# Performance work log

Hardware: AMD Instinct MI355X
Metric: run time of the kernel (lower is better)

The kernel has to match this reference:

```python
import jax, jax.numpy as jnp
import numpy as np

NUM_HEADS = 16
DIM_MODEL = 1024
DIM_K = DIM_MODEL // NUM_HEADS  # 64


def setup_inputs() -> dict:
    key = jax.random.key(0)
    ks = jax.random.split(key, 8)
    B, S, D = 2, 2048, DIM_MODEL
    scale = 1.0 / np.sqrt(D)
    return {
        "X_q": jax.random.normal(ks[0], (B, S, D), dtype=jnp.float32),
        "X_k": jax.random.normal(ks[1], (B, S, D), dtype=jnp.float32),
        "X_v": jax.random.normal(ks[2], (B, S, D), dtype=jnp.float32),
        # weights stored as [in, out] (apply as x @ W)
        "W_query": jax.random.normal(ks[3], (D, D), dtype=jnp.float32) * scale,
        "W_key": jax.random.normal(ks[4], (D, D), dtype=jnp.float32) * scale,
        "W_value": jax.random.normal(ks[5], (D, D), dtype=jnp.float32) * scale,
        "W_hidden": jax.random.normal(ks[6], (D, D), dtype=jnp.float32) * scale,
        "b_hidden": jnp.zeros((D,), dtype=jnp.float32),
    }


def _split_heads(x, B, S):
    # [B, S, D] -> [B, H, S, dk]
    return x.reshape(B, S, NUM_HEADS, DIM_K).transpose(0, 2, 1, 3)


def reference(X_q, X_k, X_v, W_query, W_key, W_value, W_hidden, b_hidden):
    B, S, D = X_q.shape
    Q = _split_heads(X_q @ W_query, B, S)
    K = _split_heads(X_k @ W_key, B, X_k.shape[1])
    V = _split_heads(X_v @ W_value, B, X_v.shape[1])
    Q = Q / np.sqrt(DIM_K).astype(np.float32)
    scores = jnp.einsum("bhqd,bhkd->bhqk", Q, K)
    A = jax.nn.sigmoid(scores)  # sigmoid attention, not softmax
    H = jnp.einsum("bhqk,bhkd->bhqd", A, V)
    # group heads: [B, H, S, dk] -> [B, S, D]
    H_cat = H.transpose(0, 2, 1, 3).reshape(B, S, D)
    H_out = H_cat @ W_hidden + b_hidden
    return (H_out, A)
```

## Files before the change

### kernel.cpp

```cpp
#include <hip/hip_runtime.h>
#include <hip/hip_bf16.h>
#include <cstddef>

typedef __bf16 bf16x8 __attribute__((ext_vector_type(8)));
typedef __bf16 bf16x4 __attribute__((ext_vector_type(4)));
typedef float f32x4 __attribute__((ext_vector_type(4)));

#define MFMA16(a, b, c) __builtin_amdgcn_mfma_f32_16x16x32_bf16((a), (b), (c), 0, 0, 0)

__global__ __launch_bounds__(256) void cvt3(const float* __restrict__ a,
                                            const float* __restrict__ b,
                                            const float* __restrict__ c,
                                            __bf16* __restrict__ oa,
                                            __bf16* __restrict__ ob,
                                            __bf16* __restrict__ oc) {
  const float* src = blockIdx.y == 0 ? a : (blockIdx.y == 1 ? b : c);
  __bf16* dst = blockIdx.y == 0 ? oa : (blockIdx.y == 1 ? ob : oc);
  const size_t i = ((size_t)blockIdx.x * 256 + threadIdx.x) * 4;
  float4 v = *(const float4*)(src + i);
  bf16x4 o = {(__bf16)v.x, (__bf16)v.y, (__bf16)v.z, (__bf16)v.w};
  *(bf16x4*)(dst + i) = o;
}

__global__ __launch_bounds__(256) void twt(const float* __restrict__ w0, const float* __restrict__ w1,
                                           const float* __restrict__ w2, const float* __restrict__ w3,
                                           __bf16* __restrict__ o0, __bf16* __restrict__ o1,
                                           __bf16* __restrict__ o2, __bf16* __restrict__ o3) {
  const float* W;
  __bf16* O;
  switch (blockIdx.z) {
    case 0: W = w0; O = o0; break;
    case 1: W = w1; O = o1; break;
    case 2: W = w2; O = o2; break;
    default: W = w3; O = o3; break;
  }
  __shared__ float t[32][33];
  const int tx = threadIdx.x & 31, ty = threadIdx.x >> 5;
  const int bx = blockIdx.x * 32, by = blockIdx.y * 32;
#pragma unroll
  for (int i = 0; i < 4; ++i)
    t[ty + 8 * i][tx] = W[(size_t)(by + ty + 8 * i) * 1024 + bx + tx];
  __syncthreads();
#pragma unroll
  for (int i = 0; i < 4; ++i)
    O[(size_t)(bx + ty + 8 * i) * 1024 + by + tx] = (__bf16)t[tx][ty + 8 * i];
}

template <bool OUT_BF16>
__global__ __launch_bounds__(256) void gemm_bt(const __bf16* __restrict__ A,
                                               const __bf16* __restrict__ B,
                                               void* __restrict__ Cout,
                                               const float* __restrict__ bias,
                                               float scale) {
  constexpr int K = 1024, N = 1024;
  const int tid = threadIdx.x, wave = tid >> 6, lane = tid & 63;
  const int qd = lane >> 4, ln = lane & 15;
  const int m0 = blockIdx.y * 128, n0 = blockIdx.x * 128;
  const int wr = wave >> 1, wc = wave & 1;

  __shared__ __align__(16) __bf16 sA[128][40];
  __shared__ __align__(16) __bf16 sB[128][40];

  f32x4 acc[4][4] = {};

  const int srow = tid >> 2, sch = (tid & 3) * 8;

  for (int k0 = 0; k0 < K; k0 += 32) {
    __syncthreads();
    *(bf16x8*)&sA[srow][sch]      = *(const bf16x8*)(A + (size_t)(m0 + srow) * K + k0 + sch);
    *(bf16x8*)&sA[srow + 64][sch] = *(const bf16x8*)(A + (size_t)(m0 + srow + 64) * K + k0 + sch);
    *(bf16x8*)&sB[srow][sch]      = *(const bf16x8*)(B + (size_t)(n0 + srow) * K + k0 + sch);
    *(bf16x8*)&sB[srow + 64][sch] = *(const bf16x8*)(B + (size_t)(n0 + srow + 64) * K + k0 + sch);
    __syncthreads();

    bf16x8 af[4], bfv[4];
#pragma unroll
    for (int i = 0; i < 4; ++i) af[i] = *(const bf16x8*)&sA[wr * 64 + i * 16 + ln][qd * 8];
#pragma unroll
    for (int j = 0; j < 4; ++j) bfv[j] = *(const bf16x8*)&sB[wc * 64 + j * 16 + ln][qd * 8];
#pragma unroll
    for (int i = 0; i < 4; ++i)
#pragma unroll
      for (int j = 0; j < 4; ++j) acc[i][j] = MFMA16(af[i], bfv[j], acc[i][j]);
  }

#pragma unroll
  for (int i = 0; i < 4; ++i)
#pragma unroll
    for (int j = 0; j < 4; ++j)
#pragma unroll
      for (int r = 0; r < 4; ++r) {
        const int row = m0 + wr * 64 + i * 16 + qd * 4 + r;
        const int col = n0 + wc * 64 + j * 16 + ln;
        float v = acc[i][j][r] * scale;
        if (bias) v += bias[col];
        if (OUT_BF16)
          ((__bf16*)Cout)[(size_t)row * N + col] = (__bf16)v;
        else
          ((float*)Cout)[(size_t)row * N + col] = v;
      }
}

__global__ __launch_bounds__(256) void attn(const __bf16* __restrict__ Q,
                                            const __bf16* __restrict__ Kb,
                                            const __bf16* __restrict__ Vb,
                                            float* __restrict__ Aout,
                                            __bf16* __restrict__ Hc) {
  const int qt = blockIdx.x, h = blockIdx.y, b = blockIdx.z;
  const int tid = threadIdx.x, wave = tid >> 6, lane = tid & 63;
  const int qd = lane >> 4, ln = lane & 15;
  const int q0 = qt * 64;
  const int wr = wave >> 1, wc = wave & 1;

  __shared__ __align__(16) __bf16 sVt[64][132];
  __shared__ __align__(16) __bf16 sKA[128 * 72];

  const __bf16* Qg = Q + (size_t)(b * 2048 + q0) * 1024 + h * 64;
  bf16x8 qf[2][2];
#pragma unroll
  for (int i = 0; i < 2; ++i)
#pragma unroll
    for (int s = 0; s < 2; ++s)
      qf[i][s] = *(const bf16x8*)(Qg + (size_t)(wr * 32 + i * 16 + ln) * 1024 + s * 32 + qd * 8);

  f32x4 hacc[4] = {};
  float* Ag = Aout + ((size_t)((b * 16 + h) * 2048 + q0)) * 2048;

  for (int kt = 0; kt < 16; ++kt) {
    const int k0 = kt * 128;
    __syncthreads();

    const __bf16* Kg = Kb + (size_t)(b * 2048 + k0) * 1024 + h * 64;
    const __bf16* Vg = Vb + (size_t)(b * 2048 + k0) * 1024 + h * 64;
#pragma unroll
    for (int p = 0; p < 4; ++p) {
      const int idx = p * 256 + tid, row = idx >> 3, ch = (idx & 7) * 8;
      *(bf16x8*)&sKA[row * 72 + ch] = *(const bf16x8*)(Kg + (size_t)row * 1024 + ch);
      bf16x8 v = *(const bf16x8*)(Vg + (size_t)row * 1024 + ch);
#pragma unroll
      for (int e = 0; e < 8; ++e) sVt[ch + e][row] = v[e];
    }
    __syncthreads();

    f32x4 sacc[2][4] = {};
#pragma unroll
    for (int ks = 0; ks < 64; ks += 32) {
      bf16x8 bfv[4];
#pragma unroll
      for (int j = 0; j < 4; ++j)
        bfv[j] = *(const bf16x8*)&sKA[(wc * 64 + j * 16 + ln) * 72 + ks + qd * 8];
#pragma unroll
      for (int i = 0; i < 2; ++i)
#pragma unroll
        for (int j = 0; j < 4; ++j) sacc[i][j] = MFMA16(qf[i][ks / 32], bfv[j], sacc[i][j]);
    }
    __syncthreads();

#pragma unroll
    for (int i = 0; i < 2; ++i)
#pragma unroll
      for (int j = 0; j < 4; ++j)
#pragma unroll
        for (int r = 0; r < 4; ++r) {
          const float s = sacc[i][j][r];
          const float a = 1.0f / (1.0f + __expf(-s));
          const int rr = wr * 32 + i * 16 + qd * 4 + r;
          const int cc = wc * 64 + j * 16 + ln;
          Ag[(size_t)rr * 2048 + k0 + cc] = a;
          sKA[rr * 136 + cc] = (__bf16)a;
        }
    __syncthreads();

#pragma unroll
    for (int ks = 0; ks < 128; ks += 32) {
      bf16x8 pa = *(const bf16x8*)&sKA[(wave * 16 + ln) * 136 + ks + qd * 8];
#pragma unroll
      for (int j = 0; j < 4; ++j) {
        const __bf16* vp = &sVt[j * 16 + ln][ks + qd * 8];
        bf16x4 lo = *(const bf16x4*)vp;
        bf16x4 hi = *(const bf16x4*)(vp + 4);
        bf16x8 bv;
#pragma unroll
        for (int e = 0; e < 4; ++e) { bv[e] = lo[e]; bv[e + 4] = hi[e]; }
        hacc[j] = MFMA16(pa, bv, hacc[j]);
      }
    }
  }

  __bf16* Hg = Hc + (size_t)(b * 2048 + q0) * 1024 + h * 64;
#pragma unroll
  for (int j = 0; j < 4; ++j)
#pragma unroll
    for (int r = 0; r < 4; ++r)
      Hg[(size_t)(wave * 16 + qd * 4 + r) * 1024 + j * 16 + ln] = (__bf16)hacc[j][r];
}

extern "C" void kernel_launch(void* const* d_in, const int* in_sizes, int n_in,
                              void* d_out, int out_size, void* d_ws, size_t ws_size,
                              hipStream_t stream) {
  const float* Xq = (const float*)d_in[0];
  const float* Xk = (const float*)d_in[1];
  const float* Xv = (const float*)d_in[2];
  const float* Wq = (const float*)d_in[3];
  const float* Wk = (const float*)d_in[4];
  const float* Wv = (const float*)d_in[5];
  const float* Wh = (const float*)d_in[6];
  const float* bh = (const float*)d_in[7];

  float* Hout = (float*)d_out;
  float* Aout = Hout + (size_t)4096 * 1024;

  __bf16* p = (__bf16*)d_ws;
  __bf16* Xq_bf = p; p += (size_t)4096 * 1024;
  __bf16* Xk_bf = p; p += (size_t)4096 * 1024;
  __bf16* Xv_bf = p; p += (size_t)4096 * 1024;
  __bf16* WqT = p; p += (size_t)1024 * 1024;
  __bf16* WkT = p; p += (size_t)1024 * 1024;
  __bf16* WvT = p; p += (size_t)1024 * 1024;
  __bf16* WhT = p; p += (size_t)1024 * 1024;
  __bf16* Qb = p; p += (size_t)4096 * 1024;
  __bf16* Kb = p; p += (size_t)4096 * 1024;
  __bf16* Vb = p; p += (size_t)4096 * 1024;
  __bf16* Hc = p; p += (size_t)4096 * 1024;

  cvt3<<<dim3(4096, 3), 256, 0, stream>>>(Xq, Xk, Xv, Xq_bf, Xk_bf, Xv_bf);
  twt<<<dim3(32, 32, 4), 256, 0, stream>>>(Wq, Wk, Wv, Wh, WqT, WkT, WvT, WhT);

  gemm_bt<true><<<dim3(8, 32), 256, 0, stream>>>(Xq_bf, WqT, (void*)Qb, nullptr, 0.125f);
  gemm_bt<true><<<dim3(8, 32), 256, 0, stream>>>(Xk_bf, WkT, (void*)Kb, nullptr, 1.0f);
  gemm_bt<true><<<dim3(8, 32), 256, 0, stream>>>(Xv_bf, WvT, (void*)Vb, nullptr, 1.0f);

  attn<<<dim3(32, 16, 2), 256, 0, stream>>>(Qb, Kb, Vb, Aout, Hc);

  gemm_bt<false><<<dim3(8, 32), 256, 0, stream>>>(Hc, WhT, (void*)Hout, bh, 1.0f);
}
```

Baseline: 909.5 us.

## Batch QKV projections into one launch with 64x128 tiles and K-step 64

```diff
diff --git a/kernel.cpp b/kernel.cpp
--- a/kernel.cpp
+++ b/kernel.cpp
@@ -47,50 +47,57 @@
 }
 
 template <bool OUT_BF16>
-__global__ __launch_bounds__(256) void gemm_bt(const __bf16* __restrict__ A,
-                                               const __bf16* __restrict__ B,
-                                               void* __restrict__ Cout,
-                                               const float* __restrict__ bias,
-                                               float scale) {
+__device__ __forceinline__ void gemm64_body(const __bf16* __restrict__ A,
+                                            const __bf16* __restrict__ B,
+                                            void* __restrict__ Cout,
+                                            const float* __restrict__ bias,
+                                            float scale) {
   constexpr int K = 1024, N = 1024;
   const int tid = threadIdx.x, wave = tid >> 6, lane = tid & 63;
   const int qd = lane >> 4, ln = lane & 15;
-  const int m0 = blockIdx.y * 128, n0 = blockIdx.x * 128;
-  const int wr = wave >> 1, wc = wave & 1;
-
-  __shared__ __align__(16) __bf16 sA[128][40];
-  __shared__ __align__(16) __bf16 sB[128][40];
-
-  f32x4 acc[4][4] = {};
-
-  const int srow = tid >> 2, sch = (tid & 3) * 8;
-
-  for (int k0 = 0; k0 < K; k0 += 32) {
-    __syncthreads();
-    *(bf16x8*)&sA[srow][sch]      = *(const bf16x8*)(A + (size_t)(m0 + srow) * K + k0 + sch);
-    *(bf16x8*)&sA[srow + 64][sch] = *(const bf16x8*)(A + (size_t)(m0 + srow + 64) * K + k0 + sch);
-    *(bf16x8*)&sB[srow][sch]      = *(const bf16x8*)(B + (size_t)(n0 + srow) * K + k0 + sch);
-    *(bf16x8*)&sB[srow + 64][sch] = *(const bf16x8*)(B + (size_t)(n0 + srow + 64) * K + k0 + sch);
-    __syncthreads();
-
-    bf16x8 af[4], bfv[4];
-#pragma unroll
-    for (int i = 0; i < 4; ++i) af[i] = *(const bf16x8*)&sA[wr * 64 + i * 16 + ln][qd * 8];
-#pragma unroll
-    for (int j = 0; j < 4; ++j) bfv[j] = *(const bf16x8*)&sB[wc * 64 + j * 16 + ln][qd * 8];
-#pragma unroll
-    for (int i = 0; i < 4; ++i)
-#pragma unroll
-      for (int j = 0; j < 4; ++j) acc[i][j] = MFMA16(af[i], bfv[j], acc[i][j]);
-  }
-
-#pragma unroll
-  for (int i = 0; i < 4; ++i)
+  const int m0 = blockIdx.y * 64, n0 = blockIdx.x * 128;
+  const int wr = wave & 1, wc = wave >> 1;
+
+  __shared__ __align__(16) __bf16 sA[64][72];
+  __shared__ __align__(16) __bf16 sB[128][72];
+
+  f32x4 acc[2][4] = {};
+
+  const int sr = tid >> 2, sc = (tid & 3) * 8;
+
+  for (int k0 = 0; k0 < K; k0 += 64) {
+    __syncthreads();
+    *(bf16x8*)&sA[sr][sc]      = *(const bf16x8*)(A + (size_t)(m0 + sr) * K + k0 + sc);
+    *(bf16x8*)&sA[sr][sc + 32] = *(const bf16x8*)(A + (size_t)(m0 + sr) * K + k0 + sc + 32);
+#pragma unroll
+    for (int h = 0; h < 128; h += 64)
+#pragma unroll
+      for (int c = 0; c < 64; c += 32)
+        *(bf16x8*)&sB[sr + h][sc + c] =
+            *(const bf16x8*)(B + (size_t)(n0 + sr + h) * K + k0 + sc + c);
+    __syncthreads();
+
+#pragma unroll
+    for (int ks = 0; ks < 64; ks += 32) {
+      bf16x8 af[2], bfv[4];
+#pragma unroll
+      for (int i = 0; i < 2; ++i) af[i] = *(const bf16x8*)&sA[wr * 32 + i * 16 + ln][ks + qd * 8];
+#pragma unroll
+      for (int j = 0; j < 4; ++j) bfv[j] = *(const bf16x8*)&sB[wc * 64 + j * 16 + ln][ks + qd * 8];
+#pragma unroll
+      for (int i = 0; i < 2; ++i)
+#pragma unroll
+        for (int j = 0; j < 4; ++j) acc[i][j] = MFMA16(af[i], bfv[j], acc[i][j]);
+    }
+  }
+
+#pragma unroll
+  for (int i = 0; i < 2; ++i)
 #pragma unroll
     for (int j = 0; j < 4; ++j)
 #pragma unroll
       for (int r = 0; r < 4; ++r) {
-        const int row = m0 + wr * 64 + i * 16 + qd * 4 + r;
+        const int row = m0 + wr * 32 + i * 16 + qd * 4 + r;
         const int col = n0 + wc * 64 + j * 16 + ln;
         float v = acc[i][j][r] * scale;
         if (bias) v += bias[col];
@@ -99,6 +106,33 @@
         else
           ((float*)Cout)[(size_t)row * N + col] = v;
       }
+}
+
+__global__ __launch_bounds__(256) void gemm_qkv(const __bf16* __restrict__ Xq,
+                                                const __bf16* __restrict__ Xk,
+                                                const __bf16* __restrict__ Xv,
+                                                const __bf16* __restrict__ WqT,
+                                                const __bf16* __restrict__ WkT,
+                                                const __bf16* __restrict__ WvT,
+                                                __bf16* __restrict__ Qb,
+                                                __bf16* __restrict__ Kb,
+                                                __bf16* __restrict__ Vb) {
+  const __bf16 *A, *B;
+  __bf16* O;
+  float sc;
+  switch (blockIdx.z) {
+    case 0: A = Xq; B = WqT; O = Qb; sc = 0.125f; break;
+    case 1: A = Xk; B = WkT; O = Kb; sc = 1.0f; break;
+    default: A = Xv; B = WvT; O = Vb; sc = 1.0f; break;
+  }
+  gemm64_body<true>(A, B, (void*)O, nullptr, sc);
+}
+
+__global__ __launch_bounds__(256) void gemm_h(const __bf16* __restrict__ Hc,
+                                              const __bf16* __restrict__ WhT,
+                                              float* __restrict__ Hout,
+                                              const float* __restrict__ bh) {
+  gemm64_body<false>(Hc, WhT, (void*)Hout, bh, 1.0f);
 }
 
 __global__ __launch_bounds__(256) void attn(const __bf16* __restrict__ Q,
@@ -226,11 +260,9 @@
   cvt3<<<dim3(4096, 3), 256, 0, stream>>>(Xq, Xk, Xv, Xq_bf, Xk_bf, Xv_bf);
   twt<<<dim3(32, 32, 4), 256, 0, stream>>>(Wq, Wk, Wv, Wh, WqT, WkT, WvT, WhT);
 
-  gemm_bt<true><<<dim3(8, 32), 256, 0, stream>>>(Xq_bf, WqT, (void*)Qb, nullptr, 0.125f);
-  gemm_bt<true><<<dim3(8, 32), 256, 0, stream>>>(Xk_bf, WkT, (void*)Kb, nullptr, 1.0f);
-  gemm_bt<true><<<dim3(8, 32), 256, 0, stream>>>(Xv_bf, WvT, (void*)Vb, nullptr, 1.0f);
+  gemm_qkv<<<dim3(8, 64, 3), 256, 0, stream>>>(Xq_bf, Xk_bf, Xv_bf, WqT, WkT, WvT, Qb, Kb, Vb);
 
   attn<<<dim3(32, 16, 2), 256, 0, stream>>>(Qb, Kb, Vb, Aout, Hc);
 
-  gemm_bt<false><<<dim3(8, 32), 256, 0, stream>>>(Hc, WhT, (void*)Hout, bh, 1.0f);
-}
+  gemm_h<<<dim3(8, 64), 256, 0, stream>>>(Hc, WhT, Hout, bh);
+}
```

New measurement: 866.2 us. 4.8% less time.
